# Optimization experiments

Measured on AMD Instinct MI355X. Metric: run time of the kernel, lower is better.

Reference implementation:

```python
import jax, jax.numpy as jnp
import numpy as np


def reference(key, value, time_decay, time_first):
    # key, value: [B, T, H]; time_decay/time_first: [H]
    u = time_first
    w = -jnp.exp(time_decay)
    B, T, H = key.shape

    def step(carry, kv):
        a, b, exponent = carry  # each [B, H]
        kt, vt = kv             # [B, H] each
        # numerically stabilized WKV output at this timestep
        max_e = jnp.maximum(exponent, u + kt)
        wt = jnp.exp(u + kt - max_e)
        scale = jnp.exp(exponent - max_e)
        wkv = (a * scale + wt * vt) / (b * scale + wt)
        # state update with decay w
        max_e2 = jnp.maximum(exponent + w, kt)
        s1 = jnp.exp(exponent + w - max_e2)
        s2 = jnp.exp(kt - max_e2)
        a_new = s1 * a + s2 * vt
        b_new = s1 * b + s2
        return (a_new, b_new, max_e2), wkv

    init = (
        jnp.zeros((B, H), dtype=key.dtype),
        jnp.zeros((B, H), dtype=key.dtype),
        jnp.full((B, H), -jnp.inf, dtype=key.dtype),
    )
    k_t = jnp.transpose(key, (1, 0, 2))    # [T, B, H]
    v_t = jnp.transpose(value, (1, 0, 2))  # [T, B, H]
    _, out = jax.lax.scan(step, init, (k_t, v_t))
    return jnp.transpose(out, (1, 0, 2))   # [B, T, H]


def setup_inputs() -> dict:
    k = jax.random.key(0)
    k1, k2, k3, k4 = jax.random.split(k, 4)
    B, T, H = 8, 2048, 768
    return {
        "key": jax.random.normal(k1, (B, T, H), dtype=jnp.float32),
        "value": jax.random.normal(k2, (B, T, H), dtype=jnp.float32),
        "time_decay": jax.random.normal(k3, (H,), dtype=jnp.float32),
        "time_first": jax.random.normal(k4, (H,), dtype=jnp.float32),
    }
```

## Files before the change

### kernel.cpp

```cpp
#include <hip/hip_runtime.h>
#include <math.h>


#define B_   8
#define T_   2048
#define H_   768
#define TPB_ 192

__device__ __forceinline__ float rcp_f(float x) { return __builtin_amdgcn_rcpf(x); }

template <int NC>
__global__ __launch_bounds__(TPB_) void wkv_phase1(
    const float* __restrict__ key, const float* __restrict__ val,
    const float* __restrict__ time_decay, float4* __restrict__ ws)
{
    constexpr int L = T_ / NC;
    const int h0 = threadIdx.x * 4;
    const int c = blockIdx.x, b = blockIdx.y;

    const float4 td = *(const float4*)(time_decay + h0);
    const float w[4] = { -__expf(td.x), -__expf(td.y), -__expf(td.z), -__expf(td.w) };

    const size_t base = ((size_t)b * T_ + (size_t)c * L) * (H_ / 4) + (h0 >> 2);
    const float4* kp = (const float4*)key + base;
    const float4* vp = (const float4*)val + base;

    float a[4] = {0.f, 0.f, 0.f, 0.f};
    float bb[4] = {0.f, 0.f, 0.f, 0.f};
    float e[4] = {-INFINITY, -INFINITY, -INFINITY, -INFINITY};

    float4 kt = kp[0], vt = vp[0];
#pragma unroll 4
    for (int t = 0; t < L; ++t) {
        float4 kn, vn;
        if (t + 1 < L) {
            kn = kp[(size_t)(t + 1) * (H_ / 4)];
            vn = vp[(size_t)(t + 1) * (H_ / 4)];
        }
        const float kk[4] = {kt.x, kt.y, kt.z, kt.w};
        const float vv[4] = {vt.x, vt.y, vt.z, vt.w};
#pragma unroll
        for (int j = 0; j < 4; ++j) {
            const float ew = e[j] + w[j];
            const float m2 = fmaxf(ew, kk[j]);
            const float s1 = __expf(ew - m2);
            const float s2 = __expf(kk[j] - m2);
            a[j]  = fmaf(s1, a[j],  s2 * vv[j]);
            bb[j] = fmaf(s1, bb[j], s2);
            e[j]  = m2;
        }
        kt = kn; vt = vn;
    }

    const size_t off = ((size_t)b * NC + c) * H_ + h0;
#pragma unroll
    for (int j = 0; j < 4; ++j)
        ws[off + j] = make_float4(a[j], bb[j], e[j], 0.f);
}

template <int NC, int P>
__global__ __launch_bounds__(256) void wkv_phase2(
    float4* __restrict__ ws, const float* __restrict__ time_decay)
{
    constexpr int L = T_ / NC;
    const int idx = blockIdx.x * 256 + threadIdx.x;
    const int b = idx / H_;
    const int h = idx - b * H_;

    const float wL = -__expf(time_decay[h]) * (float)L;

    const size_t off0 = (size_t)b * NC * H_ + h;
    float4 ring[P];
#pragma unroll
    for (int p = 0; p < P; ++p) ring[p] = ws[off0 + (size_t)p * H_];

    float ra = 0.f, rb = 0.f, re = -INFINITY;
#pragma unroll 8
    for (int c = 0; c < NC; ++c) {
        const float4 cur = ring[c & (P - 1)];
        if (c + P < NC) ring[c & (P - 1)] = ws[off0 + (size_t)(c + P) * H_];
        ws[off0 + (size_t)c * H_] = make_float4(ra, rb, re, 0.f);

        const float e1 = re + wL;
        const float m  = fmaxf(e1, cur.z);
        const float p_ = __expf(e1 - m);
        const float q_ = __expf(cur.z - m);
        ra = fmaf(ra, p_, cur.x * q_);
        rb = fmaf(rb, p_, cur.y * q_);
        re = m;
    }
}

template <int NC>
__global__ __launch_bounds__(TPB_) void wkv_phase3(
    const float* __restrict__ key, const float* __restrict__ val,
    const float* __restrict__ time_decay, const float* __restrict__ time_first,
    const float4* __restrict__ ws, float* __restrict__ out)
{
    constexpr int L = T_ / NC;
    const int h0 = threadIdx.x * 4;
    const int c = blockIdx.x, b = blockIdx.y;

    const float4 td = *(const float4*)(time_decay + h0);
    const float4 tf = *(const float4*)(time_first + h0);
    const float w[4] = { -__expf(td.x), -__expf(td.y), -__expf(td.z), -__expf(td.w) };
    const float u[4] = { tf.x, tf.y, tf.z, tf.w };

    const size_t soff = ((size_t)b * NC + c) * H_ + h0;
    float a[4], bb[4], e[4];
#pragma unroll
    for (int j = 0; j < 4; ++j) {
        const float4 s = ws[soff + j];
        a[j] = s.x; bb[j] = s.y; e[j] = s.z;
    }

    const size_t base = ((size_t)b * T_ + (size_t)c * L) * (H_ / 4) + (h0 >> 2);
    const float4* kp = (const float4*)key + base;
    const float4* vp = (const float4*)val + base;
    float4*       op = (float4*)out + base;

    float4 kt = kp[0], vt = vp[0];
#pragma unroll 4
    for (int t = 0; t < L; ++t) {
        float4 kn, vn;
        if (t + 1 < L) {
            kn = kp[(size_t)(t + 1) * (H_ / 4)];
            vn = vp[(size_t)(t + 1) * (H_ / 4)];
        }
        const float kk[4] = {kt.x, kt.y, kt.z, kt.w};
        const float vv[4] = {vt.x, vt.y, vt.z, vt.w};
        float o[4];
#pragma unroll
        for (int j = 0; j < 4; ++j) {
            const float uk = u[j] + kk[j];
            const float m1 = fmaxf(e[j], uk);
            const float wt = __expf(uk - m1);
            const float sc = __expf(e[j] - m1);
            const float num = fmaf(a[j],  sc, wt * vv[j]);
            const float den = fmaf(bb[j], sc, wt);
            o[j] = num * rcp_f(den);

            const float ew = e[j] + w[j];
            const float m2 = fmaxf(ew, kk[j]);
            const float s1 = __expf(ew - m2);
            const float s2 = __expf(kk[j] - m2);
            a[j]  = fmaf(s1, a[j],  s2 * vv[j]);
            bb[j] = fmaf(s1, bb[j], s2);
            e[j]  = m2;
        }
        op[(size_t)t * (H_ / 4)] = make_float4(o[0], o[1], o[2], o[3]);
        kt = kn; vt = vn;
    }
}

template <int NC>
static void launch_all(const float* key, const float* val, const float* td,
                       const float* tf, float* out, float4* ws, hipStream_t stream)
{
    dim3 blk13(TPB_);
    dim3 grid13(NC, B_);
    wkv_phase1<NC><<<grid13, blk13, 0, stream>>>(key, val, td, ws);

    dim3 grid2((B_ * H_) / 256);
    wkv_phase2<NC, 8><<<grid2, dim3(256), 0, stream>>>(ws, td);

    wkv_phase3<NC><<<grid13, blk13, 0, stream>>>(key, val, td, tf, ws, out);
}

extern "C" void kernel_launch(void* const* d_in, const int* in_sizes, int n_in,
                              void* d_out, int out_size, void* d_ws, size_t ws_size,
                              hipStream_t stream) {
    const float* key = (const float*)d_in[0];
    const float* val = (const float*)d_in[1];
    const float* td  = (const float*)d_in[2];
    const float* tf  = (const float*)d_in[3];
    float* out = (float*)d_out;
    float4* ws = (float4*)d_ws;

    const size_t need128 = (size_t)B_ * 128 * H_ * sizeof(float4);
    const size_t need64  = (size_t)B_ * 64  * H_ * sizeof(float4);
    const size_t need32  = (size_t)B_ * 32  * H_ * sizeof(float4);

    if (ws_size >= need128)      launch_all<128>(key, val, td, tf, out, ws, stream);
    else if (ws_size >= need64)  launch_all<64>(key, val, td, tf, out, ws, stream);
    else if (ws_size >= need32)  launch_all<32>(key, val, td, tf, out, ws, stream);
    else                         launch_all<16>(key, val, td, tf, out, ws, stream);
}
```

Before: 176.7 us.

## Split chunk-state workspace into SoA arrays and deepen load prefetch

After: 212.6 us. 20.3% more time.

```diff
diff --git a/kernel.cpp b/kernel.cpp
--- a/kernel.cpp
+++ b/kernel.cpp
@@ -5,6 +5,7 @@
 #define B_   8
 #define T_   2048
 #define H_   768
+#define HV4_ (H_ / 4)
 #define TPB_ 192
 
 __device__ __forceinline__ float rcp_f(float x) { return __builtin_amdgcn_rcpf(x); }
@@ -12,30 +13,39 @@
 template <int NC>
 __global__ __launch_bounds__(TPB_) void wkv_phase1(
     const float* __restrict__ key, const float* __restrict__ val,
-    const float* __restrict__ time_decay, float4* __restrict__ ws)
+    const float* __restrict__ time_decay,
+    float* __restrict__ wa, float* __restrict__ wb, float* __restrict__ we)
 {
     constexpr int L = T_ / NC;
+    constexpr int D = 4;
     const int h0 = threadIdx.x * 4;
     const int c = blockIdx.x, b = blockIdx.y;
 
     const float4 td = *(const float4*)(time_decay + h0);
     const float w[4] = { -__expf(td.x), -__expf(td.y), -__expf(td.z), -__expf(td.w) };
 
-    const size_t base = ((size_t)b * T_ + (size_t)c * L) * (H_ / 4) + (h0 >> 2);
+    const size_t base = ((size_t)b * T_ + (size_t)c * L) * HV4_ + threadIdx.x;
     const float4* kp = (const float4*)key + base;
     const float4* vp = (const float4*)val + base;
+
+    float4 kbuf[D], vbuf[D];
+#pragma unroll
+    for (int i = 0; i < D; ++i) {
+        kbuf[i] = kp[(size_t)i * HV4_];
+        vbuf[i] = vp[(size_t)i * HV4_];
+    }
 
     float a[4] = {0.f, 0.f, 0.f, 0.f};
     float bb[4] = {0.f, 0.f, 0.f, 0.f};
     float e[4] = {-INFINITY, -INFINITY, -INFINITY, -INFINITY};
 
-    float4 kt = kp[0], vt = vp[0];
-#pragma unroll 4
+#pragma unroll
     for (int t = 0; t < L; ++t) {
-        float4 kn, vn;
-        if (t + 1 < L) {
-            kn = kp[(size_t)(t + 1) * (H_ / 4)];
-            vn = vp[(size_t)(t + 1) * (H_ / 4)];
+        const float4 kt = kbuf[t & (D - 1)];
+        const float4 vt = vbuf[t & (D - 1)];
+        if (t + D < L) {
+            kbuf[t & (D - 1)] = kp[(size_t)(t + D) * HV4_];
+            vbuf[t & (D - 1)] = vp[(size_t)(t + D) * HV4_];
         }
         const float kk[4] = {kt.x, kt.y, kt.z, kt.w};
         const float vv[4] = {vt.x, vt.y, vt.z, vt.w};
@@ -49,18 +59,18 @@
             bb[j] = fmaf(s1, bb[j], s2);
             e[j]  = m2;
         }
-        kt = kn; vt = vn;
-    }
-
-    const size_t off = ((size_t)b * NC + c) * H_ + h0;
-#pragma unroll
-    for (int j = 0; j < 4; ++j)
-        ws[off + j] = make_float4(a[j], bb[j], e[j], 0.f);
+    }
+
+    const size_t off = (((size_t)b * NC + c) * H_ + h0) >> 2;
+    ((float4*)wa)[off] = make_float4(a[0], a[1], a[2], a[3]);
+    ((float4*)wb)[off] = make_float4(bb[0], bb[1], bb[2], bb[3]);
+    ((float4*)we)[off] = make_float4(e[0], e[1], e[2], e[3]);
 }
 
 template <int NC, int P>
 __global__ __launch_bounds__(256) void wkv_phase2(
-    float4* __restrict__ ws, const float* __restrict__ time_decay)
+    float* __restrict__ wa, float* __restrict__ wb, float* __restrict__ we,
+    const float* __restrict__ time_decay)
 {
     constexpr int L = T_ / NC;
     const int idx = blockIdx.x * 256 + threadIdx.x;
@@ -70,23 +80,32 @@
     const float wL = -__expf(time_decay[h]) * (float)L;
 
     const size_t off0 = (size_t)b * NC * H_ + h;
-    float4 ring[P];
-#pragma unroll
-    for (int p = 0; p < P; ++p) ring[p] = ws[off0 + (size_t)p * H_];
+    float ca[P], cb[P], ce[P];
+#pragma unroll
+    for (int p = 0; p < P; ++p) {
+        ca[p] = wa[off0 + (size_t)p * H_];
+        cb[p] = wb[off0 + (size_t)p * H_];
+        ce[p] = we[off0 + (size_t)p * H_];
+    }
 
     float ra = 0.f, rb = 0.f, re = -INFINITY;
-#pragma unroll 8
+#pragma unroll 16
     for (int c = 0; c < NC; ++c) {
-        const float4 cur = ring[c & (P - 1)];
-        if (c + P < NC) ring[c & (P - 1)] = ws[off0 + (size_t)(c + P) * H_];
-        ws[off0 + (size_t)c * H_] = make_float4(ra, rb, re, 0.f);
+        const int s = c & (P - 1);
+        const float xa = ca[s], xb = cb[s], xe = ce[s];
+        if (c + P < NC) {
+            const size_t noff = off0 + (size_t)(c + P) * H_;
+            ca[s] = wa[noff]; cb[s] = wb[noff]; ce[s] = we[noff];
+        }
+        const size_t coff = off0 + (size_t)c * H_;
+        wa[coff] = ra; wb[coff] = rb; we[coff] = re;
 
         const float e1 = re + wL;
-        const float m  = fmaxf(e1, cur.z);
+        const float m  = fmaxf(e1, xe);
         const float p_ = __expf(e1 - m);
-        const float q_ = __expf(cur.z - m);
-        ra = fmaf(ra, p_, cur.x * q_);
-        rb = fmaf(rb, p_, cur.y * q_);
+        const float q_ = __expf(xe - m);
+        ra = fmaf(ra, p_, xa * q_);
+        rb = fmaf(rb, p_, xb * q_);
         re = m;
     }
 }
@@ -95,9 +114,11 @@
 __global__ __launch_bounds__(TPB_) void wkv_phase3(
     const float* __restrict__ key, const float* __restrict__ val,
     const float* __restrict__ time_decay, const float* __restrict__ time_first,
-    const float4* __restrict__ ws, float* __restrict__ out)
+    const float* __restrict__ wa, const float* __restrict__ wb,
+    const float* __restrict__ we, float* __restrict__ out)
 {
     constexpr int L = T_ / NC;
+    constexpr int D = 4;
     const int h0 = threadIdx.x * 4;
     const int c = blockIdx.x, b = blockIdx.y;
 
@@ -106,26 +127,33 @@
     const float w[4] = { -__expf(td.x), -__expf(td.y), -__expf(td.z), -__expf(td.w) };
     const float u[4] = { tf.x, tf.y, tf.z, tf.w };
 
-    const size_t soff = ((size_t)b * NC + c) * H_ + h0;
-    float a[4], bb[4], e[4];
-#pragma unroll
-    for (int j = 0; j < 4; ++j) {
-        const float4 s = ws[soff + j];
-        a[j] = s.x; bb[j] = s.y; e[j] = s.z;
-    }
-
-    const size_t base = ((size_t)b * T_ + (size_t)c * L) * (H_ / 4) + (h0 >> 2);
+    const size_t soff = (((size_t)b * NC + c) * H_ + h0) >> 2;
+    const float4 sa = ((const float4*)wa)[soff];
+    const float4 sb = ((const float4*)wb)[soff];
+    const float4 se = ((const float4*)we)[soff];
+    float a[4]  = {sa.x, sa.y, sa.z, sa.w};
+    float bb[4] = {sb.x, sb.y, sb.z, sb.w};
+    float e[4]  = {se.x, se.y, se.z, se.w};
+
+    const size_t base = ((size_t)b * T_ + (size_t)c * L) * HV4_ + threadIdx.x;
     const float4* kp = (const float4*)key + base;
     const float4* vp = (const float4*)val + base;
     float4*       op = (float4*)out + base;
 
-    float4 kt = kp[0], vt = vp[0];
-#pragma unroll 4
+    float4 kbuf[D], vbuf[D];
+#pragma unroll
+    for (int i = 0; i < D; ++i) {
+        kbuf[i] = kp[(size_t)i * HV4_];
+        vbuf[i] = vp[(size_t)i * HV4_];
+    }
+
+#pragma unroll
     for (int t = 0; t < L; ++t) {
-        float4 kn, vn;
-        if (t + 1 < L) {
-            kn = kp[(size_t)(t + 1) * (H_ / 4)];
-            vn = vp[(size_t)(t + 1) * (H_ / 4)];
+        const float4 kt = kbuf[t & (D - 1)];
+        const float4 vt = vbuf[t & (D - 1)];
+        if (t + D < L) {
+            kbuf[t & (D - 1)] = kp[(size_t)(t + D) * HV4_];
+            vbuf[t & (D - 1)] = vp[(size_t)(t + D) * HV4_];
         }
         const float kk[4] = {kt.x, kt.y, kt.z, kt.w};
         const float vv[4] = {vt.x, vt.y, vt.z, vt.w};
@@ -148,23 +176,25 @@
             bb[j] = fmaf(s1, bb[j], s2);
             e[j]  = m2;
         }
-        op[(size_t)t * (H_ / 4)] = make_float4(o[0], o[1], o[2], o[3]);
-        kt = kn; vt = vn;
+        op[(size_t)t * HV4_] = make_float4(o[0], o[1], o[2], o[3]);
     }
 }
 
 template <int NC>
 static void launch_all(const float* key, const float* val, const float* td,
-                       const float* tf, float* out, float4* ws, hipStream_t stream)
-{
-    dim3 blk13(TPB_);
+                       const float* tf, float* out, float* ws, hipStream_t stream)
+{
+    float* wa = ws;
+    float* wb = wa + (size_t)B_ * NC * H_;
+    float* we = wb + (size_t)B_ * NC * H_;
+
     dim3 grid13(NC, B_);
-    wkv_phase1<NC><<<grid13, blk13, 0, stream>>>(key, val, td, ws);
+    wkv_phase1<NC><<<grid13, dim3(TPB_), 0, stream>>>(key, val, td, wa, wb, we);
 
     dim3 grid2((B_ * H_) / 256);
-    wkv_phase2<NC, 8><<<grid2, dim3(256), 0, stream>>>(ws, td);
-
-    wkv_phase3<NC><<<grid13, blk13, 0, stream>>>(key, val, td, tf, ws, out);
+    wkv_phase2<NC, 16><<<grid2, dim3(256), 0, stream>>>(wa, wb, we, td);
+
+    wkv_phase3<NC><<<grid13, dim3(TPB_), 0, stream>>>(key, val, td, tf, wa, wb, we, out);
 }
 
 extern "C" void kernel_launch(void* const* d_in, const int* in_sizes, int n_in,
@@ -175,14 +205,11 @@
     const float* td  = (const float*)d_in[2];
     const float* tf  = (const float*)d_in[3];
     float* out = (float*)d_out;
-    float4* ws = (float4*)d_ws;
-
-    const size_t need128 = (size_t)B_ * 128 * H_ * sizeof(float4);
-    const size_t need64  = (size_t)B_ * 64  * H_ * sizeof(float4);
-    const size_t need32  = (size_t)B_ * 32  * H_ * sizeof(float4);
-
-    if (ws_size >= need128)      launch_all<128>(key, val, td, tf, out, ws, stream);
-    else if (ws_size >= need64)  launch_all<64>(key, val, td, tf, out, ws, stream);
-    else if (ws_size >= need32)  launch_all<32>(key, val, td, tf, out, ws, stream);
-    else                         launch_all<16>(key, val, td, tf, out, ws, stream);
-}
+    float* ws = (float*)d_ws;
+
+    const size_t needNC = (size_t)3 * B_ * H_ * sizeof(float);
+    if (ws_size >= 128 * needNC)      launch_all<128>(key, val, td, tf, out, ws, stream);
+    else if (ws_size >= 64 * needNC)  launch_all<64>(key, val, td, tf, out, ws, stream);
+    else if (ws_size >= 32 * needNC)  launch_all<32>(key, val, td, tf, out, ws, stream);
+    else                              launch_all<16>(key, val, td, tf, out, ws, stream);
+}
```

## Fuse three WKV phases into one cooperative kernel with wave-parallel chunk scan

Applied to the files above, without the earlier changes.

New measurement: 267.3 us. +51.3%, slower.

```diff
diff --git a/kernel.cpp b/kernel.cpp
--- a/kernel.cpp
+++ b/kernel.cpp
@@ -1,44 +1,66 @@
 #include <hip/hip_runtime.h>
+#include <hip/hip_cooperative_groups.h>
 #include <math.h>
+
+namespace cg = cooperative_groups;
 
 
 #define B_   8
 #define T_   2048
 #define H_   768
+#define HV4_ (H_ / 4)
 #define TPB_ 192
+#define CUS_ 256
+
+typedef float v4f __attribute__((ext_vector_type(4)));
+
+struct S3 { float a, b, e; };
+
+__device__ __forceinline__ S3 comb(const S3 x, const S3 y, float wLen) {
+    const float e1 = x.e + wLen;
+    const float m  = fmaxf(e1, y.e);
+    const float p  = __expf(e1 - m);
+    const float q  = __expf(y.e - m);
+    S3 r;
+    r.a = fmaf(x.a, p, y.a * q);
+    r.b = fmaf(x.b, p, y.b * q);
+    r.e = m;
+    return r;
+}
 
 __device__ __forceinline__ float rcp_f(float x) { return __builtin_amdgcn_rcpf(x); }
 
 template <int NC>
-__global__ __launch_bounds__(TPB_) void wkv_phase1(
+__device__ __forceinline__ void phaseA(
     const float* __restrict__ key, const float* __restrict__ val,
-    const float* __restrict__ time_decay, float4* __restrict__ ws)
+    const float* __restrict__ td, float4* __restrict__ agg4,
+    int b, int c, int tid)
 {
     constexpr int L = T_ / NC;
-    const int h0 = threadIdx.x * 4;
-    const int c = blockIdx.x, b = blockIdx.y;
-
-    const float4 td = *(const float4*)(time_decay + h0);
-    const float w[4] = { -__expf(td.x), -__expf(td.y), -__expf(td.z), -__expf(td.w) };
-
-    const size_t base = ((size_t)b * T_ + (size_t)c * L) * (H_ / 4) + (h0 >> 2);
+    constexpr int D = 4;
+    const int h0 = tid * 4;
+    const float4 tdv = *(const float4*)(td + h0);
+    const float w[4] = { -__expf(tdv.x), -__expf(tdv.y), -__expf(tdv.z), -__expf(tdv.w) };
+
+    const size_t base = ((size_t)b * T_ + (size_t)c * L) * HV4_ + tid;
     const float4* kp = (const float4*)key + base;
     const float4* vp = (const float4*)val + base;
 
-    float a[4] = {0.f, 0.f, 0.f, 0.f};
-    float bb[4] = {0.f, 0.f, 0.f, 0.f};
-    float e[4] = {-INFINITY, -INFINITY, -INFINITY, -INFINITY};
-
-    float4 kt = kp[0], vt = vp[0];
-#pragma unroll 4
+    float4 kbuf[D], vbuf[D];
+#pragma unroll
+    for (int i = 0; i < D; ++i) { kbuf[i] = kp[(size_t)i * HV4_]; vbuf[i] = vp[(size_t)i * HV4_]; }
+
+    float a[4] = {0.f,0.f,0.f,0.f}, bb[4] = {0.f,0.f,0.f,0.f};
+    float e[4] = {-INFINITY,-INFINITY,-INFINITY,-INFINITY};
+
+#pragma unroll
     for (int t = 0; t < L; ++t) {
-        float4 kn, vn;
-        if (t + 1 < L) {
-            kn = kp[(size_t)(t + 1) * (H_ / 4)];
-            vn = vp[(size_t)(t + 1) * (H_ / 4)];
-        }
-        const float kk[4] = {kt.x, kt.y, kt.z, kt.w};
-        const float vv[4] = {vt.x, vt.y, vt.z, vt.w};
+        const float4 kt = kbuf[t & (D-1)], vt = vbuf[t & (D-1)];
+        if (t + D < L) {
+            kbuf[t & (D-1)] = kp[(size_t)(t+D) * HV4_];
+            vbuf[t & (D-1)] = vp[(size_t)(t+D) * HV4_];
+        }
+        const float kk[4] = {kt.x,kt.y,kt.z,kt.w}, vv[4] = {vt.x,vt.y,vt.z,vt.w};
 #pragma unroll
         for (int j = 0; j < 4; ++j) {
             const float ew = e[j] + w[j];
@@ -49,86 +71,96 @@
             bb[j] = fmaf(s1, bb[j], s2);
             e[j]  = m2;
         }
-        kt = kn; vt = vn;
-    }
-
-    const size_t off = ((size_t)b * NC + c) * H_ + h0;
+    }
 #pragma unroll
     for (int j = 0; j < 4; ++j)
-        ws[off + j] = make_float4(a[j], bb[j], e[j], 0.f);
-}
-
-template <int NC, int P>
-__global__ __launch_bounds__(256) void wkv_phase2(
-    float4* __restrict__ ws, const float* __restrict__ time_decay)
+        agg4[((size_t)b * H_ + h0 + j) * NC + c] = make_float4(a[j], bb[j], e[j], 0.f);
+}
+
+template <int NC>
+__device__ __forceinline__ void phaseB(
+    const float4* __restrict__ agg4, float4* __restrict__ st4,
+    const float* __restrict__ td, int s, int lane)
 {
     constexpr int L = T_ / NC;
-    const int idx = blockIdx.x * 256 + threadIdx.x;
-    const int b = idx / H_;
-    const int h = idx - b * H_;
-
-    const float wL = -__expf(time_decay[h]) * (float)L;
-
-    const size_t off0 = (size_t)b * NC * H_ + h;
-    float4 ring[P];
-#pragma unroll
-    for (int p = 0; p < P; ++p) ring[p] = ws[off0 + (size_t)p * H_];
-
-    float ra = 0.f, rb = 0.f, re = -INFINITY;
-#pragma unroll 8
-    for (int c = 0; c < NC; ++c) {
-        const float4 cur = ring[c & (P - 1)];
-        if (c + P < NC) ring[c & (P - 1)] = ws[off0 + (size_t)(c + P) * H_];
-        ws[off0 + (size_t)c * H_] = make_float4(ra, rb, re, 0.f);
-
-        const float e1 = re + wL;
-        const float m  = fmaxf(e1, cur.z);
-        const float p_ = __expf(e1 - m);
-        const float q_ = __expf(cur.z - m);
-        ra = fmaf(ra, p_, cur.x * q_);
-        rb = fmaf(rb, p_, cur.y * q_);
-        re = m;
-    }
-}
-
-template <int NC>
-__global__ __launch_bounds__(TPB_) void wkv_phase3(
+    constexpr int CPL = NC / 64;
+    const int b = s / H_;
+    const int h = s - b * H_;
+    const float wL = -__expf(td[h]) * (float)L;
+    const float wP = wL * (float)CPL;
+    const size_t rb = ((size_t)b * H_ + h) * NC;
+
+    S3 x[CPL];
+#pragma unroll
+    for (int i = 0; i < CPL; ++i) {
+        const float4 t = agg4[rb + lane * CPL + i];
+        x[i].a = t.x; x[i].b = t.y; x[i].e = t.z;
+    }
+    S3 p = x[0];
+    if (CPL == 2) p = comb(x[0], x[CPL-1], wL);
+
+    S3 incl = p;
+#pragma unroll
+    for (int d = 1; d < 64; d <<= 1) {
+        S3 o;
+        o.a = __shfl_up(incl.a, d);
+        o.b = __shfl_up(incl.b, d);
+        o.e = __shfl_up(incl.e, d);
+        const S3 t = comb(o, incl, wP * (float)d);
+        if (lane >= d) incl = t;
+    }
+    S3 excl;
+    excl.a = __shfl_up(incl.a, 1);
+    excl.b = __shfl_up(incl.b, 1);
+    excl.e = __shfl_up(incl.e, 1);
+    if (lane == 0) { excl.a = 0.f; excl.b = 0.f; excl.e = -INFINITY; }
+
+    st4[rb + lane * CPL] = make_float4(excl.a, excl.b, excl.e, 0.f);
+    if (CPL == 2) {
+        const S3 in1 = comb(excl, x[0], wL);
+        st4[rb + lane * CPL + 1] = make_float4(in1.a, in1.b, in1.e, 0.f);
+    }
+}
+
+template <int NC>
+__device__ __forceinline__ void phaseC(
     const float* __restrict__ key, const float* __restrict__ val,
-    const float* __restrict__ time_decay, const float* __restrict__ time_first,
-    const float4* __restrict__ ws, float* __restrict__ out)
+    const float* __restrict__ td, const float* __restrict__ tf,
+    const float4* __restrict__ st4, float* __restrict__ out,
+    int b, int c, int tid)
 {
     constexpr int L = T_ / NC;
-    const int h0 = threadIdx.x * 4;
-    const int c = blockIdx.x, b = blockIdx.y;
-
-    const float4 td = *(const float4*)(time_decay + h0);
-    const float4 tf = *(const float4*)(time_first + h0);
-    const float w[4] = { -__expf(td.x), -__expf(td.y), -__expf(td.z), -__expf(td.w) };
-    const float u[4] = { tf.x, tf.y, tf.z, tf.w };
-
-    const size_t soff = ((size_t)b * NC + c) * H_ + h0;
+    constexpr int D = 4;
+    const int h0 = tid * 4;
+    const float4 tdv = *(const float4*)(td + h0);
+    const float4 tfv = *(const float4*)(tf + h0);
+    const float w[4] = { -__expf(tdv.x), -__expf(tdv.y), -__expf(tdv.z), -__expf(tdv.w) };
+    const float u[4] = { tfv.x, tfv.y, tfv.z, tfv.w };
+
     float a[4], bb[4], e[4];
 #pragma unroll
     for (int j = 0; j < 4; ++j) {
-        const float4 s = ws[soff + j];
+        const float4 s = st4[((size_t)b * H_ + h0 + j) * NC + c];
         a[j] = s.x; bb[j] = s.y; e[j] = s.z;
     }
 
-    const size_t base = ((size_t)b * T_ + (size_t)c * L) * (H_ / 4) + (h0 >> 2);
+    const size_t base = ((size_t)b * T_ + (size_t)c * L) * HV4_ + tid;
     const float4* kp = (const float4*)key + base;
     const float4* vp = (const float4*)val + base;
     float4*       op = (float4*)out + base;
 
-    float4 kt = kp[0], vt = vp[0];
-#pragma unroll 4
+    float4 kbuf[D], vbuf[D];
+#pragma unroll
+    for (int i = 0; i < D; ++i) { kbuf[i] = kp[(size_t)i * HV4_]; vbuf[i] = vp[(size_t)i * HV4_]; }
+
+#pragma unroll
     for (int t = 0; t < L; ++t) {
-        float4 kn, vn;
-        if (t + 1 < L) {
-            kn = kp[(size_t)(t + 1) * (H_ / 4)];
-            vn = vp[(size_t)(t + 1) * (H_ / 4)];
-        }
-        const float kk[4] = {kt.x, kt.y, kt.z, kt.w};
-        const float vv[4] = {vt.x, vt.y, vt.z, vt.w};
+        const float4 kt = kbuf[t & (D-1)], vt = vbuf[t & (D-1)];
+        if (t + D < L) {
+            kbuf[t & (D-1)] = kp[(size_t)(t+D) * HV4_];
+            vbuf[t & (D-1)] = vp[(size_t)(t+D) * HV4_];
+        }
+        const float kk[4] = {kt.x,kt.y,kt.z,kt.w}, vv[4] = {vt.x,vt.y,vt.z,vt.w};
         float o[4];
 #pragma unroll
         for (int j = 0; j < 4; ++j) {
@@ -136,9 +168,7 @@
             const float m1 = fmaxf(e[j], uk);
             const float wt = __expf(uk - m1);
             const float sc = __expf(e[j] - m1);
-            const float num = fmaf(a[j],  sc, wt * vv[j]);
-            const float den = fmaf(bb[j], sc, wt);
-            o[j] = num * rcp_f(den);
+            o[j] = fmaf(a[j], sc, wt * vv[j]) * rcp_f(fmaf(bb[j], sc, wt));
 
             const float ew = e[j] + w[j];
             const float m2 = fmaxf(ew, kk[j]);
@@ -148,23 +178,64 @@
             bb[j] = fmaf(s1, bb[j], s2);
             e[j]  = m2;
         }
-        op[(size_t)t * (H_ / 4)] = make_float4(o[0], o[1], o[2], o[3]);
-        kt = kn; vt = vn;
-    }
-}
-
-template <int NC>
-static void launch_all(const float* key, const float* val, const float* td,
-                       const float* tf, float* out, float4* ws, hipStream_t stream)
-{
-    dim3 blk13(TPB_);
-    dim3 grid13(NC, B_);
-    wkv_phase1<NC><<<grid13, blk13, 0, stream>>>(key, val, td, ws);
-
-    dim3 grid2((B_ * H_) / 256);
-    wkv_phase2<NC, 8><<<grid2, dim3(256), 0, stream>>>(ws, td);
-
-    wkv_phase3<NC><<<grid13, blk13, 0, stream>>>(key, val, td, tf, ws, out);
+        v4f ov = { o[0], o[1], o[2], o[3] };
+        __builtin_nontemporal_store(ov, (v4f*)&op[(size_t)t * HV4_]);
+    }
+}
+
+template <int NC, int MODE>
+__global__ __launch_bounds__(TPB_, 3) void wkv_kern(
+    const float* __restrict__ key, const float* __restrict__ val,
+    const float* __restrict__ td, const float* __restrict__ tf,
+    float4* __restrict__ agg4, float4* __restrict__ st4,
+    float* __restrict__ out)
+{
+    constexpr int NT = B_ * NC;
+    const int tid = threadIdx.x;
+
+    if (MODE == 0 || MODE == 1) {
+        for (int tile = blockIdx.x; tile < NT; tile += gridDim.x)
+            phaseA<NC>(key, val, td, agg4, tile / NC, tile % NC, tid);
+    }
+    if (MODE == 0) cg::this_grid().sync();
+    if (MODE == 0 || MODE == 2) {
+        const int nw   = gridDim.x * (TPB_ / 64);
+        const int wid  = blockIdx.x * (TPB_ / 64) + (tid >> 6);
+        const int lane = tid & 63;
+        for (int s = wid; s < B_ * H_; s += nw)
+            phaseB<NC>(agg4, st4, td, s, lane);
+    }
+    if (MODE == 0) cg::this_grid().sync();
+    if (MODE == 0 || MODE == 3) {
+        for (int tile = blockIdx.x; tile < NT; tile += gridDim.x)
+            phaseC<NC>(key, val, td, tf, st4, out, tile / NC, tile % NC, tid);
+    }
+}
+
+template <int NC>
+static void launch_nc(const float* key, const float* val, const float* td,
+                      const float* tf, float* out, void* ws, hipStream_t stream)
+{
+    constexpr int NT = B_ * NC;
+    float4* agg4 = (float4*)ws;
+    float4* st4  = agg4 + (size_t)B_ * H_ * NC;
+
+    int maxB = 0;
+    hipError_t qerr = hipOccupancyMaxActiveBlocksPerMultiprocessor(
+        &maxB, wkv_kern<NC, 0>, TPB_, 0);
+    if (qerr == hipSuccess && maxB > 0) {
+        int nblk = maxB * CUS_;
+        if (nblk > NT) nblk = NT;
+        void* args[7] = { (void*)&key, (void*)&val, (void*)&td, (void*)&tf,
+                          (void*)&agg4, (void*)&st4, (void*)&out };
+        hipError_t lerr = hipLaunchCooperativeKernel(
+            reinterpret_cast<void*>(wkv_kern<NC, 0>), dim3(nblk), dim3(TPB_),
+            args, 0, stream);
+        if (lerr == hipSuccess) return;
+    }
+    wkv_kern<NC, 1><<<dim3(NT), dim3(TPB_), 0, stream>>>(key, val, td, tf, agg4, st4, out);
+    wkv_kern<NC, 2><<<dim3((B_ * H_) / (TPB_ / 64)), dim3(TPB_), 0, stream>>>(key, val, td, tf, agg4, st4, out);
+    wkv_kern<NC, 3><<<dim3(NT), dim3(TPB_), 0, stream>>>(key, val, td, tf, agg4, st4, out);
 }
 
 extern "C" void kernel_launch(void* const* d_in, const int* in_sizes, int n_in,
@@ -175,14 +246,8 @@
     const float* td  = (const float*)d_in[2];
     const float* tf  = (const float*)d_in[3];
     float* out = (float*)d_out;
-    float4* ws = (float4*)d_ws;
-
-    const size_t need128 = (size_t)B_ * 128 * H_ * sizeof(float4);
-    const size_t need64  = (size_t)B_ * 64  * H_ * sizeof(float4);
-    const size_t need32  = (size_t)B_ * 32  * H_ * sizeof(float4);
-
-    if (ws_size >= need128)      launch_all<128>(key, val, td, tf, out, ws, stream);
-    else if (ws_size >= need64)  launch_all<64>(key, val, td, tf, out, ws, stream);
-    else if (ws_size >= need32)  launch_all<32>(key, val, td, tf, out, ws, stream);
-    else                         launch_all<16>(key, val, td, tf, out, ws, stream);
-}
+
+    const size_t need128 = (size_t)2 * B_ * H_ * 128 * sizeof(float4);
+    if (ws_size >= need128) launch_nc<128>(key, val, td, tf, out, d_ws, stream);
+    else                    launch_nc<64>(key, val, td, tf, out, d_ws, stream);
+}
```
